# Optimization experiments

Hardware: AMD Instinct MI355X
Metric: run time of the kernel (lower is better)

## Reference

```python
import jax, jax.numpy as jnp
import numpy as np

NEG_SLOPE = 0.2  # PyG GATConv default negative_slope


def gat_conv(x, src, dst, W, a_src, a_dst, b):
    """PyG GATConv with concat=False (mean over heads). src/dst include self-loops."""
    N = x.shape[0]
    H, C = a_src.shape
    h = (x @ W).reshape(N, H, C)                      # [N,H,C]
    alpha_src = (h * a_src).sum(-1)                   # [N,H]
    alpha_dst = (h * a_dst).sum(-1)                   # [N,H]
    e = jax.nn.leaky_relu(alpha_src[src] + alpha_dst[dst], NEG_SLOPE)  # [E,H]
    # segment softmax over incoming edges of each dst node
    emax = jax.ops.segment_max(e, dst, num_segments=N)                 # [N,H]
    ex = jnp.exp(e - emax[dst])                                        # [E,H]
    denom = jax.ops.segment_sum(ex, dst, num_segments=N)               # [N,H]
    alpha = ex / denom[dst]                                            # [E,H]
    msg = h[src] * alpha[:, :, None]                                   # [E,H,C]
    out = jax.ops.segment_sum(msg, dst, num_segments=N)                # [N,H,C]
    return out.mean(axis=1) + b                                        # concat=False -> mean heads


def setup_inputs() -> dict:
    key = jax.random.key(0)
    ks = jax.random.split(key, 16)
    N, F_IN, H, C, E = 50000, 3, 4, 64, 800000
    inp = {
        "x": jax.random.normal(ks[0], (N, F_IN), dtype=jnp.float32),
        "edge_index": jax.random.randint(ks[1], (2, E), 0, N, dtype=jnp.int32),
        "W1": jax.random.normal(ks[2], (F_IN, H * C), dtype=jnp.float32) * 0.1,
        "a1_src": jax.random.normal(ks[3], (H, C), dtype=jnp.float32) * 0.1,
        "a1_dst": jax.random.normal(ks[4], (H, C), dtype=jnp.float32) * 0.1,
        "b1": jnp.zeros((C,), dtype=jnp.float32),
        "W2": jax.random.normal(ks[5], (C, H * C), dtype=jnp.float32) * 0.1,
        "a2_src": jax.random.normal(ks[6], (H, C), dtype=jnp.float32) * 0.1,
        "a2_dst": jax.random.normal(ks[7], (H, C), dtype=jnp.float32) * 0.1,
        "b2": jnp.zeros((C,), dtype=jnp.float32),
        "W3": jax.random.normal(ks[8], (C, H * C), dtype=jnp.float32) * 0.1,
        "a3_src": jax.random.normal(ks[9], (H, C), dtype=jnp.float32) * 0.1,
        "a3_dst": jax.random.normal(ks[10], (H, C), dtype=jnp.float32) * 0.1,
        "b3": jnp.zeros((C,), dtype=jnp.float32),
        "lin_w": jax.random.normal(ks[11], (C, 1), dtype=jnp.float32) * 0.1,
        "lin_b": jnp.zeros((1,), dtype=jnp.float32),
    }
    return inp


def reference(x, edge_index, W1, a1_src, a1_dst, b1, W2, a2_src, a2_dst, b2,
              W3, a3_src, a3_dst, b3, lin_w, lin_b):
    N = x.shape[0]
    loops = jnp.arange(N, dtype=edge_index.dtype)  # PyG add_self_loops=True default
    src = jnp.concatenate([edge_index[0], loops])
    dst = jnp.concatenate([edge_index[1], loops])

    h1 = jax.nn.elu(gat_conv(x, src, dst, W1, a1_src, a1_dst, b1))
    h2 = jax.nn.elu(gat_conv(h1, src, dst, W2, a2_src, a2_dst, b2)) + h1
    h3 = jax.nn.elu(gat_conv(h2, src, dst, W3, a3_src, a3_dst, b3)) + h2
    return h3 @ lin_w + lin_b
```

## Files before the change

### kernel.cpp

```cpp
#include <hip/hip_runtime.h>
#include <math.h>

#define HEADS 4
#define CH 64
#define HC 256

typedef __attribute__((ext_vector_type(8))) short bf16x8;
typedef __attribute__((ext_vector_type(4))) float f32x4;

__device__ __forceinline__ float lrelu(float v) { return v > 0.f ? v : 0.2f * v; }

__device__ __forceinline__ unsigned int f2bf(float f) {
    unsigned int u = __float_as_uint(f);
    u += 0x7fffu + ((u >> 16) & 1u);
    return u >> 16;
}
__device__ __forceinline__ float bf2f(unsigned short u) {
    return __uint_as_float(((unsigned int)u) << 16);
}

__device__ __forceinline__ float4 wave_sum4(float4 v) {
#pragma unroll
    for (int m = 32; m; m >>= 1) {
        v.x += __shfl_xor(v.x, m);
        v.y += __shfl_xor(v.y, m);
        v.z += __shfl_xor(v.z, m);
        v.w += __shfl_xor(v.w, m);
    }
    return v;
}

__global__ void count_kernel(const int* __restrict__ dst, int E, int vec_ok,
                             float scale8, int* __restrict__ deg) {
    int r = blockIdx.x & 7;
    int i = (blockIdx.x >> 3) * blockDim.x + threadIdx.x;
    int e0 = i * 4;
    if (e0 >= E) return;
    int d[4];
    int cnt;
    if (vec_ok && e0 + 3 < E) {
        int4 v = *(const int4*)(dst + e0);
        d[0] = v.x; d[1] = v.y; d[2] = v.z; d[3] = v.w; cnt = 4;
    } else {
        cnt = min(4, E - e0);
        for (int k = 0; k < cnt; ++k) d[k] = dst[e0 + k];
    }
    for (int k = 0; k < cnt; ++k) {
        int rr = min(7, (int)((float)d[k] * scale8));
        if (rr == r) atomicAdd(&deg[d[k]], 1);
    }
}

__global__ void scan_blocks(const int* __restrict__ deg,
                            int* __restrict__ off,
                            int* __restrict__ bsum,
                            const float* __restrict__ x,
                            float4* __restrict__ xq, int N) {
    __shared__ int sh[256];
    int t = threadIdx.x;
    int g = blockIdx.x * 256 + t;
    int v = (g < N) ? deg[g] + 1 : 0;
    if (g < N) xq[g] = make_float4(x[3 * g], x[3 * g + 1], x[3 * g + 2], 0.f);
    sh[t] = v;
    __syncthreads();
    for (int d = 1; d < 256; d <<= 1) {
        int xv = (t >= d) ? sh[t - d] : 0;
        __syncthreads();
        sh[t] += xv;
        __syncthreads();
    }
    if (g < N) off[g] = sh[t] - v;
    if (t == 255) bsum[blockIdx.x] = sh[255];
}

__global__ void scan_bsums(int* __restrict__ bsum, int G,
                           int* __restrict__ total_out) {
    __shared__ int sh[256];
    int t = threadIdx.x;
    int chunk = (G + 255) / 256;
    int lo = t * chunk, hi = min(lo + chunk, G);
    int s = 0;
    for (int i = lo; i < hi; ++i) s += bsum[i];
    sh[t] = s;
    __syncthreads();
    for (int d = 1; d < 256; d <<= 1) {
        int xv = (t >= d) ? sh[t - d] : 0;
        __syncthreads();
        sh[t] += xv;
        __syncthreads();
    }
    int run = (t > 0) ? sh[t - 1] : 0;
    for (int i = lo; i < hi; ++i) { int v = bsum[i]; bsum[i] = run; run += v; }
    if (t == 255) *total_out = sh[255];
}

__global__ void scan_add(int* __restrict__ off, const int* __restrict__ bsum,
                         const int* __restrict__ deg,
                         int* __restrict__ csr_src, int N) {
    int g = blockIdx.x * 256 + threadIdx.x;
    if (g < N) {
        int o = off[g] + bsum[blockIdx.x];
        off[g] = o;
        csr_src[o + deg[g]] = g;
    }
}

__global__ void scatter_kernel(const int* __restrict__ src,
                               const int* __restrict__ dst, int E, int vec_ok,
                               float scale8,
                               const int* __restrict__ off,
                               int* __restrict__ cursor,
                               int* __restrict__ csr_src) {
    int r = blockIdx.x & 7;
    int i = (blockIdx.x >> 3) * blockDim.x + threadIdx.x;
    int e0 = i * 4;
    if (e0 >= E) return;
    int s[4], d[4];
    int cnt;
    if (vec_ok && e0 + 3 < E) {
        int4 sv = *(const int4*)(src + e0);
        int4 dv = *(const int4*)(dst + e0);
        s[0] = sv.x; s[1] = sv.y; s[2] = sv.z; s[3] = sv.w;
        d[0] = dv.x; d[1] = dv.y; d[2] = dv.z; d[3] = dv.w; cnt = 4;
    } else {
        cnt = min(4, E - e0);
        for (int k = 0; k < cnt; ++k) { s[k] = src[e0 + k]; d[k] = dst[e0 + k]; }
    }
    for (int k = 0; k < cnt; ++k) {
        int rr = min(7, (int)((float)d[k] * scale8));
        if (rr != r) continue;
        int p = atomicAdd(&cursor[d[k]], 1);
        csr_src[off[d[k]] + p] = s[k];
    }
}

__device__ __forceinline__ void prep_blk(int b, int t, const float* W,
                                         const float* a_s, const float* a_d,
                                         unsigned short* Wb, float* ws,
                                         float* wd) {
    if (b < 64) {
        Wb[b * 256 + t] = (unsigned short)f2bf(W[(t >> 2) * HC + (t & 3) * CH + b]);
    } else {
        int idx = (b - 64) * 256 + t;
        int which = idx >= 256;
        int i = which ? idx - 256 : idx;
        int k = i >> 2, h = i & 3;
        const float* av = (which ? a_d : a_s) + h * CH;
        const float* Wr = W + (size_t)k * HC + h * CH;
        float s = 0.f;
        for (int c = 0; c < CH; ++c) s += Wr[c] * av[c];
        (which ? wd : ws)[i] = s;
    }
}

__global__ void prep_all(const float* __restrict__ W1,
                         const float* __restrict__ a1s,
                         const float* __restrict__ a1d,
                         float* __restrict__ ws1, float* __restrict__ wd1,
                         const float* __restrict__ W2,
                         const float* __restrict__ a2s,
                         const float* __restrict__ a2d,
                         unsigned short* __restrict__ Wb2,
                         float* __restrict__ ws2, float* __restrict__ wd2,
                         const float* __restrict__ W3,
                         const float* __restrict__ a3s,
                         const float* __restrict__ a3d,
                         unsigned short* __restrict__ Wb3,
                         float* __restrict__ ws3, float* __restrict__ wd3) {
    int b = blockIdx.x, t = threadIdx.x;
    if (b < 66) {
        prep_blk(b, t, W2, a2s, a2d, Wb2, ws2, wd2);
    } else if (b < 132) {
        prep_blk(b - 66, t, W3, a3s, a3d, Wb3, ws3, wd3);
    } else {
        for (int idx = t; idx < 24; idx += blockDim.x) {
            int which = idx >= 12;
            int i = which ? idx - 12 : idx;
            int k = i >> 2, h = i & 3;
            const float* av = (which ? a1d : a1s) + h * CH;
            const float* Wr = W1 + (size_t)k * HC + h * CH;
            float s = 0.f;
            for (int c = 0; c < CH; ++c) s += Wr[c] * av[c];
            (which ? wd1 : ws1)[i] = s;
        }
    }
}

__global__ void agg_kernel(const int* __restrict__ off,
                           const int* __restrict__ csr_src,
                           const unsigned short* __restrict__ xp,
                           const float4* __restrict__ asrc4,
                           const float4* __restrict__ adst4,
                           uint2* __restrict__ zb2, int N) {
    __shared__ float4 exs[4][64];
    __shared__ unsigned int sss[4][64];
    int node = (blockIdx.x * blockDim.x + threadIdx.x) >> 6;
    int w = (threadIdx.x >> 6) & 3;
    int lane = threadIdx.x & 63;
    if (node >= N) return;
    int o0 = off[node], o1 = off[node + 1];
    int deg = o1 - o0;
    float4 ad = adst4[node];

    float l0 = 0.f, l1 = 0.f, l2 = 0.f, l3 = 0.f;
    float z0 = 0.f, z1 = 0.f, z2 = 0.f, z3 = 0.f;
    const char* xpb = (const char*)xp + lane * 2;

    for (int base = 0; base < deg; base += 64) {
        int i = base + lane;
        int s = 0;
        float4 ev = make_float4(-INFINITY, -INFINITY, -INFINITY, -INFINITY);
        if (i < deg) {
            s = csr_src[o0 + i];
            float4 as = asrc4[s];
            ev.x = lrelu(as.x + ad.x);
            ev.y = lrelu(as.y + ad.y);
            ev.z = lrelu(as.z + ad.z);
            ev.w = lrelu(as.w + ad.w);
        }
        float4 ex;
        ex.x = __expf(ev.x);
        ex.y = __expf(ev.y);
        ex.z = __expf(ev.z);
        ex.w = __expf(ev.w);
        float4 ls = wave_sum4(ex);
        l0 += ls.x; l1 += ls.y; l2 += ls.z; l3 += ls.w;
        exs[w][lane] = ex;
        sss[w][lane] = (unsigned)s * 128u;

        int cnt = min(64, deg - base);
#pragma unroll 4
        for (int e = 0; e < cnt; ++e) {
            unsigned soff = sss[w][e];
            float4 exe = exs[w][e];
            float xk = bf2f(*(const unsigned short*)(xpb + soff));
            z0 += exe.x * xk; z1 += exe.y * xk;
            z2 += exe.z * xk; z3 += exe.w * xk;
        }
    }
    float s0 = 0.25f / l0, s1 = 0.25f / l1, s2 = 0.25f / l2, s3 = 0.25f / l3;
    uint2 zo;
    zo.x = f2bf(z0 * s0) | (f2bf(z1 * s1) << 16);
    zo.y = f2bf(z2 * s2) | (f2bf(z3 * s3) << 16);
    zb2[(size_t)node * CH + lane] = zo;
}

__global__ void gemm_mfma(const unsigned short* __restrict__ zb,
                          const unsigned short* __restrict__ Wb,
                          const float* __restrict__ bias,
                          const float* __restrict__ residual,
                          const float4* __restrict__ wsn4,
                          const float4* __restrict__ wdn4,
                          float4* __restrict__ asrc4,
                          float4* __restrict__ adst4,
                          const float* __restrict__ lin_w,
                          const float* __restrict__ lin_b,
                          float* __restrict__ out_f32,
                          unsigned short* __restrict__ out_pack,
                          float* __restrict__ out_final, int N) {
    int w = threadIdx.x >> 6;
    int lane = threadIdx.x & 63;
    int quad = lane >> 4, col = lane & 15;
    int nbase = blockIdx.x * 64 + w * 16;

    f32x4 zero4 = {0.f, 0.f, 0.f, 0.f};
    f32x4 acc[4];
#pragma unroll
    for (int t = 0; t < 4; ++t) acc[t] = zero4;

    const unsigned short* arow = zb + (size_t)(nbase + col) * HC + quad * 8;
#pragma unroll
    for (int q = 0; q < 8; ++q) {
        bf16x8 af = *(const bf16x8*)(arow + q * 32);
#pragma unroll
        for (int t = 0; t < 4; ++t) {
            const unsigned short* bp = Wb + (size_t)(t * 16 + col) * HC + q * 32 + quad * 8;
            bf16x8 bfrag = *(const bf16x8*)bp;
            acc[t] = __builtin_amdgcn_mfma_f32_16x16x32_bf16(af, bfrag, acc[t], 0, 0, 0);
        }
    }

    if (!out_final) {
        float vv[4][4];
#pragma unroll
        for (int t = 0; t < 4; ++t) {
            int c = t * 16 + col;
            float bc = bias[c];
#pragma unroll
            for (int r = 0; r < 4; ++r) {
                int n = nbase + quad * 4 + r;
                float v = acc[t][r] + bc;
                v = v > 0.f ? v : expm1f(v);
                v += residual[(size_t)n * CH + c];
                vv[t][r] = v;
                if (n < N) {
                    out_f32[(size_t)n * CH + c] = v;
                    out_pack[(size_t)n * CH + c] = (unsigned short)f2bf(v);
                }
            }
        }
        float4 wsv[4], wdv[4];
#pragma unroll
        for (int t = 0; t < 4; ++t) { wsv[t] = wsn4[t * 16 + col]; wdv[t] = wdn4[t * 16 + col]; }
#pragma unroll
        for (int r = 0; r < 4; ++r) {
            int n = nbase + quad * 4 + r;
            float4 sa = make_float4(0.f, 0.f, 0.f, 0.f);
            float4 da = make_float4(0.f, 0.f, 0.f, 0.f);
#pragma unroll
            for (int t = 0; t < 4; ++t) {
                float v = vv[t][r];
                sa.x += v * wsv[t].x; sa.y += v * wsv[t].y;
                sa.z += v * wsv[t].z; sa.w += v * wsv[t].w;
                da.x += v * wdv[t].x; da.y += v * wdv[t].y;
                da.z += v * wdv[t].z; da.w += v * wdv[t].w;
            }
#pragma unroll
            for (int m = 8; m; m >>= 1) {
                sa.x += __shfl_xor(sa.x, m); sa.y += __shfl_xor(sa.y, m);
                sa.z += __shfl_xor(sa.z, m); sa.w += __shfl_xor(sa.w, m);
                da.x += __shfl_xor(da.x, m); da.y += __shfl_xor(da.y, m);
                da.z += __shfl_xor(da.z, m); da.w += __shfl_xor(da.w, m);
            }
            if (col == 0 && n < N) { asrc4[n] = sa; adst4[n] = da; }
        }
    } else {
        float lw[4], bb[4];
#pragma unroll
        for (int t = 0; t < 4; ++t) { lw[t] = lin_w[t * 16 + col]; bb[t] = bias[t * 16 + col]; }
#pragma unroll
        for (int r = 0; r < 4; ++r) {
            int n = nbase + quad * 4 + r;
            float ts = 0.f;
#pragma unroll
            for (int t = 0; t < 4; ++t) {
                float v = acc[t][r] + bb[t];
                v = v > 0.f ? v : expm1f(v);
                v += residual[(size_t)n * CH + (t * 16 + col)];
                ts += v * lw[t];
            }
            ts += __shfl_xor(ts, 1);
            ts += __shfl_xor(ts, 2);
            ts += __shfl_xor(ts, 4);
            ts += __shfl_xor(ts, 8);
            if (col == 0 && n < N) out_final[n] = ts + lin_b[0];
        }
    }
}

__global__ void fused1_kernel(const int* __restrict__ off,
                              const int* __restrict__ csr_src,
                              const float4* __restrict__ xq,
                              const float* __restrict__ ws,
                              const float* __restrict__ wd,
                              float4* __restrict__ zl, int N) {
    int t = blockIdx.x * blockDim.x + threadIdx.x;
    int n = t >> 2, j = t & 3;
    if (n >= N) return;
    float4 xn = xq[n];
    float ad0 = xn.x * wd[0] + xn.y * wd[4] + xn.z * wd[8];
    float ad1 = xn.x * wd[1] + xn.y * wd[5] + xn.z * wd[9];
    float ad2 = xn.x * wd[2] + xn.y * wd[6] + xn.z * wd[10];
    float ad3 = xn.x * wd[3] + xn.y * wd[7] + xn.z * wd[11];

    int o0 = off[n], o1 = off[n + 1];
    float z[12];
#pragma unroll
    for (int q = 0; q < 12; ++q) z[q] = 0.f;
    float l0 = 0.f, l1 = 0.f, l2 = 0.f, l3 = 0.f;

    for (int i = o0 + j; i < o1; i += 4) {
        int s = csr_src[i];
        float4 xv = xq[s];
        float e0 = __expf(lrelu(xv.x * ws[0] + xv.y * ws[4] + xv.z * ws[8]  + ad0));
        float e1 = __expf(lrelu(xv.x * ws[1] + xv.y * ws[5] + xv.z * ws[9]  + ad1));
        float e2 = __expf(lrelu(xv.x * ws[2] + xv.y * ws[6] + xv.z * ws[10] + ad2));
        float e3 = __expf(lrelu(xv.x * ws[3] + xv.y * ws[7] + xv.z * ws[11] + ad3));
        l0 += e0; l1 += e1; l2 += e2; l3 += e3;
        z[0] += e0 * xv.x; z[1]  += e0 * xv.y; z[2]  += e0 * xv.z;
        z[3] += e1 * xv.x; z[4]  += e1 * xv.y; z[5]  += e1 * xv.z;
        z[6] += e2 * xv.x; z[7]  += e2 * xv.y; z[8]  += e2 * xv.z;
        z[9] += e3 * xv.x; z[10] += e3 * xv.y; z[11] += e3 * xv.z;
    }
#pragma unroll
    for (int m = 1; m < 4; m <<= 1) {
#pragma unroll
        for (int q = 0; q < 12; ++q) z[q] += __shfl_xor(z[q], m);
        l0 += __shfl_xor(l0, m);
        l1 += __shfl_xor(l1, m);
        l2 += __shfl_xor(l2, m);
        l3 += __shfl_xor(l3, m);
    }
    if (j == 0) {
        zl[(size_t)n * 4 + 0] = make_float4(z[0], z[1], z[2], z[3]);
        zl[(size_t)n * 4 + 1] = make_float4(z[4], z[5], z[6], z[7]);
        zl[(size_t)n * 4 + 2] = make_float4(z[8], z[9], z[10], z[11]);
        zl[(size_t)n * 4 + 3] = make_float4(l0, l1, l2, l3);
    }
}

__global__ void epi1_kernel(const float4* __restrict__ zl,
                            const float* __restrict__ W1,
                            const float* __restrict__ b1,
                            const float4* __restrict__ ws2_4,
                            const float4* __restrict__ wd2_4,
                            float4* __restrict__ asrc4,
                            float4* __restrict__ adst4,
                            float* __restrict__ out,
                            unsigned short* __restrict__ out_pack, int N) {
    int node = (blockIdx.x * blockDim.x + threadIdx.x) >> 6;
    int c = threadIdx.x & 63;
    if (node >= N) return;
    float4 z0 = zl[(size_t)node * 4 + 0];
    float4 z1 = zl[(size_t)node * 4 + 1];
    float4 z2 = zl[(size_t)node * 4 + 2];
    float4 l4 = zl[(size_t)node * 4 + 3];
    float i0 = 0.25f / l4.x, i1 = 0.25f / l4.y;
    float i2 = 0.25f / l4.z, i3 = 0.25f / l4.w;
    float acc =
        (z0.x * W1[0 * HC +   0 + c] + z0.y * W1[1 * HC +   0 + c] + z0.z * W1[2 * HC +   0 + c]) * i0 +
        (z0.w * W1[0 * HC +  64 + c] + z1.x * W1[1 * HC +  64 + c] + z1.y * W1[2 * HC +  64 + c]) * i1 +
        (z1.z * W1[0 * HC + 128 + c] + z1.w * W1[1 * HC + 128 + c] + z2.x * W1[2 * HC + 128 + c]) * i2 +
        (z2.y * W1[0 * HC + 192 + c] + z2.z * W1[1 * HC + 192 + c] + z2.w * W1[2 * HC + 192 + c]) * i3;
    float v = acc + b1[c];
    v = v > 0.f ? v : expm1f(v);
    out[(size_t)node * CH + c] = v;
    out_pack[(size_t)node * CH + c] = (unsigned short)f2bf(v);
    float4 wsv = ws2_4[c], wdv = wd2_4[c];
    float4 sacc = make_float4(v * wsv.x, v * wsv.y, v * wsv.z, v * wsv.w);
    float4 dacc = make_float4(v * wdv.x, v * wdv.y, v * wdv.z, v * wdv.w);
    sacc = wave_sum4(sacc);
    dacc = wave_sum4(dacc);
    if (c == 0) { asrc4[node] = sacc; adst4[node] = dacc; }
}

extern "C" void kernel_launch(void* const* d_in, const int* in_sizes, int n_in,
                              void* d_out, int out_size, void* d_ws, size_t ws_size,
                              hipStream_t stream) {
    const float* x      = (const float*)d_in[0];
    const int*   ei     = (const int*)  d_in[1];
    const float* W1     = (const float*)d_in[2];
    const float* a1s    = (const float*)d_in[3];
    const float* a1d    = (const float*)d_in[4];
    const float* b1     = (const float*)d_in[5];
    const float* W2     = (const float*)d_in[6];
    const float* a2s    = (const float*)d_in[7];
    const float* a2d    = (const float*)d_in[8];
    const float* b2     = (const float*)d_in[9];
    const float* W3     = (const float*)d_in[10];
    const float* a3s    = (const float*)d_in[11];
    const float* a3d    = (const float*)d_in[12];
    const float* b3     = (const float*)d_in[13];
    const float* lin_w  = (const float*)d_in[14];
    const float* lin_b  = (const float*)d_in[15];

    const int N = in_sizes[0] / 3;
    const int E = in_sizes[1] / 2;
    const int Et = E + N;
    const int* src = ei;
    const int* dst = ei + E;
    const float scale8 = 8.0f / (float)N;
    const int vec_ok = ((((size_t)src | (size_t)dst) & 15) == 0) ? 1 : 0;

    float* xq_f   = (float*)d_ws;
    unsigned short* zb  = (unsigned short*)(xq_f + (size_t)N * 4);
    unsigned short* xpA = zb  + (size_t)N * HC;
    unsigned short* xpB = xpA + (size_t)N * CH;
    unsigned short* Wb2 = xpB + (size_t)N * CH;
    unsigned short* Wb3 = Wb2 + 16384;
    float* bufA   = (float*)(Wb3 + 16384);
    float* bufB   = bufA + (size_t)N * CH;
    float* zl     = bufB + (size_t)N * CH;
    float* asrc   = zl   + (size_t)N * 16;
    float* adst   = asrc + (size_t)N * 4;
    float* ws1    = adst + (size_t)N * 4;
    float* wd1    = ws1 + 16;
    float* ws2    = wd1 + 16;
    float* wd2    = ws2 + 256;
    float* ws3    = wd2 + 256;
    float* wd3    = ws3 + 256;
    int* deg      = (int*)(wd3 + 256);
    int* cursor   = deg + N;
    int* off      = cursor + N;
    int* bsum     = off + N + 4;
    int* csr_src  = bsum + 256;

    const int B = 256;
    const int G = (N + 255) / 256;
    const int EB4 = (E + 3) / 4;
    const int CB = (EB4 + B - 1) / B;

    hipMemsetAsync(deg, 0, (size_t)2 * N * sizeof(int), stream);
    count_kernel<<<CB * 8, B, 0, stream>>>(dst, E, vec_ok, scale8, deg);
    scan_blocks<<<G, B, 0, stream>>>(deg, off, bsum, x, (float4*)xq_f, N);
    scan_bsums<<<1, B, 0, stream>>>(bsum, G, off + N);
    scan_add<<<G, B, 0, stream>>>(off, bsum, deg, csr_src, N);
    scatter_kernel<<<CB * 8, B, 0, stream>>>(src, dst, E, vec_ok, scale8,
                                             off, cursor, csr_src);

    prep_all<<<133, B, 0, stream>>>(W1, a1s, a1d, ws1, wd1,
                                    W2, a2s, a2d, Wb2, ws2, wd2,
                                    W3, a3s, a3d, Wb3, ws3, wd3);

    int nwave_blocks = (N * 64 + B - 1) / B;
    int ngemm_blocks = (N + 63) / 64;

    fused1_kernel<<<(N * 4 + B - 1) / B, B, 0, stream>>>(
        off, csr_src, (const float4*)xq_f, ws1, wd1, (float4*)zl, N);
    epi1_kernel<<<nwave_blocks, B, 0, stream>>>(
        (const float4*)zl, W1, b1, (const float4*)ws2, (const float4*)wd2,
        (float4*)asrc, (float4*)adst, bufA, xpA, N);

    agg_kernel<<<nwave_blocks, B, 0, stream>>>(
        off, csr_src, xpA, (const float4*)asrc, (const float4*)adst,
        (uint2*)zb, N);
    gemm_mfma<<<ngemm_blocks, B, 0, stream>>>(
        zb, Wb2, b2, bufA, (const float4*)ws3, (const float4*)wd3,
        (float4*)asrc, (float4*)adst,
        nullptr, nullptr, bufB, xpB, nullptr, N);

    agg_kernel<<<nwave_blocks, B, 0, stream>>>(
        off, csr_src, xpB, (const float4*)asrc, (const float4*)adst,
        (uint2*)zb, N);
    gemm_mfma<<<ngemm_blocks, B, 0, stream>>>(
        zb, Wb3, b3, bufB, nullptr, nullptr, nullptr, nullptr,
        lin_w, lin_b, nullptr, nullptr, (float*)d_out, N);
}
```

Before: 344.5 us.

## Record edge slots during counting and split aggregation across half-waves

The count pass now stores each edge's atomic return value as its slot. The scatter becomes a single atomic-free pass with no per-range filtering, which removes the second round of atomics and the 8x replicated edge reads. The aggregation kernel now has each half-wave handle alternate edges, with each lane loading two bf16 features as one 32-bit word, and the halves are combined with a cross-half shuffle before a 16-byte store. This costs an extra E-sized slot buffer and more registers per lane in the aggregation.

```diff
diff --git a/kernel.cpp b/kernel.cpp
--- a/kernel.cpp
+++ b/kernel.cpp
@@ -31,7 +31,8 @@
 }
 
 __global__ void count_kernel(const int* __restrict__ dst, int E, int vec_ok,
-                             float scale8, int* __restrict__ deg) {
+                             float scale8, int* __restrict__ deg,
+                             int* __restrict__ slot) {
     int r = blockIdx.x & 7;
     int i = (blockIdx.x >> 3) * blockDim.x + threadIdx.x;
     int e0 = i * 4;
@@ -47,7 +48,7 @@
     }
     for (int k = 0; k < cnt; ++k) {
         int rr = min(7, (int)((float)d[k] * scale8));
-        if (rr == r) atomicAdd(&deg[d[k]], 1);
+        if (rr == r) slot[e0 + k] = atomicAdd(&deg[d[k]], 1);
     }
 }
 
@@ -105,32 +106,28 @@
     }
 }
 
-__global__ void scatter_kernel(const int* __restrict__ src,
-                               const int* __restrict__ dst, int E, int vec_ok,
-                               float scale8,
-                               const int* __restrict__ off,
-                               int* __restrict__ cursor,
-                               int* __restrict__ csr_src) {
-    int r = blockIdx.x & 7;
-    int i = (blockIdx.x >> 3) * blockDim.x + threadIdx.x;
+__global__ void scatter_plain(const int* __restrict__ src,
+                              const int* __restrict__ dst,
+                              const int* __restrict__ slot, int E, int vec_ok,
+                              const int* __restrict__ off,
+                              int* __restrict__ csr_src) {
+    int i = blockIdx.x * blockDim.x + threadIdx.x;
     int e0 = i * 4;
     if (e0 >= E) return;
-    int s[4], d[4];
-    int cnt;
     if (vec_ok && e0 + 3 < E) {
         int4 sv = *(const int4*)(src + e0);
         int4 dv = *(const int4*)(dst + e0);
-        s[0] = sv.x; s[1] = sv.y; s[2] = sv.z; s[3] = sv.w;
-        d[0] = dv.x; d[1] = dv.y; d[2] = dv.z; d[3] = dv.w; cnt = 4;
+        int4 pv = *(const int4*)(slot + e0);
+        csr_src[off[dv.x] + pv.x] = sv.x;
+        csr_src[off[dv.y] + pv.y] = sv.y;
+        csr_src[off[dv.z] + pv.z] = sv.z;
+        csr_src[off[dv.w] + pv.w] = sv.w;
     } else {
-        cnt = min(4, E - e0);
-        for (int k = 0; k < cnt; ++k) { s[k] = src[e0 + k]; d[k] = dst[e0 + k]; }
-    }
-    for (int k = 0; k < cnt; ++k) {
-        int rr = min(7, (int)((float)d[k] * scale8));
-        if (rr != r) continue;
-        int p = atomicAdd(&cursor[d[k]], 1);
-        csr_src[off[d[k]] + p] = s[k];
+        int cnt = min(4, E - e0);
+        for (int k = 0; k < cnt; ++k) {
+            int e = e0 + k;
+            csr_src[off[dst[e]] + slot[e]] = src[e];
+        }
     }
 }
 
@@ -191,20 +188,24 @@
                            const unsigned short* __restrict__ xp,
                            const float4* __restrict__ asrc4,
                            const float4* __restrict__ adst4,
-                           uint2* __restrict__ zb2, int N) {
+                           unsigned short* __restrict__ zb, int N) {
     __shared__ float4 exs[4][64];
     __shared__ unsigned int sss[4][64];
     int node = (blockIdx.x * blockDim.x + threadIdx.x) >> 6;
     int w = (threadIdx.x >> 6) & 3;
     int lane = threadIdx.x & 63;
     if (node >= N) return;
+    int half = lane >> 5;
+    int lk = lane & 31;
     int o0 = off[node], o1 = off[node + 1];
     int deg = o1 - o0;
     float4 ad = adst4[node];
 
     float l0 = 0.f, l1 = 0.f, l2 = 0.f, l3 = 0.f;
-    float z0 = 0.f, z1 = 0.f, z2 = 0.f, z3 = 0.f;
-    const char* xpb = (const char*)xp + lane * 2;
+    float z[8];
+#pragma unroll
+    for (int q = 0; q < 8; ++q) z[q] = 0.f;
+    const char* xpb2 = (const char*)xp + lk * 4;
 
     for (int base = 0; base < deg; base += 64) {
         int i = base + lane;
@@ -229,20 +230,32 @@
         sss[w][lane] = (unsigned)s * 128u;
 
         int cnt = min(64, deg - base);
-#pragma unroll 4
-        for (int e = 0; e < cnt; ++e) {
+#pragma unroll 2
+        for (int e2 = 0; e2 < cnt; e2 += 2) {
+            int e = e2 + half;
             unsigned soff = sss[w][e];
             float4 exe = exs[w][e];
-            float xk = bf2f(*(const unsigned short*)(xpb + soff));
-            z0 += exe.x * xk; z1 += exe.y * xk;
-            z2 += exe.z * xk; z3 += exe.w * xk;
-        }
-    }
+            unsigned xx = *(const unsigned*)(xpb2 + soff);
+            float xk0 = bf2f((unsigned short)(xx & 0xffffu));
+            float xk1 = bf2f((unsigned short)(xx >> 16));
+            z[0] += exe.x * xk0; z[1] += exe.y * xk0;
+            z[2] += exe.z * xk0; z[3] += exe.w * xk0;
+            z[4] += exe.x * xk1; z[5] += exe.y * xk1;
+            z[6] += exe.z * xk1; z[7] += exe.w * xk1;
+        }
+    }
+#pragma unroll
+    for (int q = 0; q < 8; ++q) z[q] += __shfl_xor(z[q], 32);
+
     float s0 = 0.25f / l0, s1 = 0.25f / l1, s2 = 0.25f / l2, s3 = 0.25f / l3;
-    uint2 zo;
-    zo.x = f2bf(z0 * s0) | (f2bf(z1 * s1) << 16);
-    zo.y = f2bf(z2 * s2) | (f2bf(z3 * s3) << 16);
-    zb2[(size_t)node * CH + lane] = zo;
+    if (half == 0) {
+        uint4 zo;
+        zo.x = f2bf(z[0] * s0) | (f2bf(z[1] * s1) << 16);
+        zo.y = f2bf(z[2] * s2) | (f2bf(z[3] * s3) << 16);
+        zo.z = f2bf(z[4] * s0) | (f2bf(z[5] * s1) << 16);
+        zo.w = f2bf(z[6] * s2) | (f2bf(z[7] * s3) << 16);
+        *(uint4*)((char*)zb + (size_t)node * 512 + lk * 16) = zo;
+    }
 }
 
 __global__ void gemm_mfma(const unsigned short* __restrict__ zb,
@@ -480,23 +493,22 @@
     float* ws3    = wd2 + 256;
     float* wd3    = ws3 + 256;
     int* deg      = (int*)(wd3 + 256);
-    int* cursor   = deg + N;
-    int* off      = cursor + N;
+    int* off      = deg + N;
     int* bsum     = off + N + 4;
-    int* csr_src  = bsum + 256;
+    int* slot     = bsum + 256;
+    int* csr_src  = slot + E;
 
     const int B = 256;
     const int G = (N + 255) / 256;
     const int EB4 = (E + 3) / 4;
     const int CB = (EB4 + B - 1) / B;
 
-    hipMemsetAsync(deg, 0, (size_t)2 * N * sizeof(int), stream);
-    count_kernel<<<CB * 8, B, 0, stream>>>(dst, E, vec_ok, scale8, deg);
+    hipMemsetAsync(deg, 0, (size_t)N * sizeof(int), stream);
+    count_kernel<<<CB * 8, B, 0, stream>>>(dst, E, vec_ok, scale8, deg, slot);
     scan_blocks<<<G, B, 0, stream>>>(deg, off, bsum, x, (float4*)xq_f, N);
     scan_bsums<<<1, B, 0, stream>>>(bsum, G, off + N);
     scan_add<<<G, B, 0, stream>>>(off, bsum, deg, csr_src, N);
-    scatter_kernel<<<CB * 8, B, 0, stream>>>(src, dst, E, vec_ok, scale8,
-                                             off, cursor, csr_src);
+    scatter_plain<<<CB, B, 0, stream>>>(src, dst, slot, E, vec_ok, off, csr_src);
 
     prep_all<<<133, B, 0, stream>>>(W1, a1s, a1d, ws1, wd1,
                                     W2, a2s, a2d, Wb2, ws2, wd2,
@@ -513,7 +525,7 @@
 
     agg_kernel<<<nwave_blocks, B, 0, stream>>>(
         off, csr_src, xpA, (const float4*)asrc, (const float4*)adst,
-        (uint2*)zb, N);
+        zb, N);
     gemm_mfma<<<ngemm_blocks, B, 0, stream>>>(
         zb, Wb2, b2, bufA, (const float4*)ws3, (const float4*)wd3,
         (float4*)asrc, (float4*)adst,
@@ -521,7 +533,7 @@
 
     agg_kernel<<<nwave_blocks, B, 0, stream>>>(
         off, csr_src, xpB, (const float4*)asrc, (const float4*)adst,
-        (uint2*)zb, N);
+        zb, N);
     gemm_mfma<<<ngemm_blocks, B, 0, stream>>>(
         zb, Wb3, b3, bufB, nullptr, nullptr, nullptr, nullptr,
         lin_w, lin_b, nullptr, nullptr, (float*)d_out, N);
```

Result: faster. 319.8 us (-7.2%).
